# Kernel tuning notes

Measured on AMD Instinct MI355X. Metric: run time of the kernel, lower is better.

## Reference

```python
import jax, jax.numpy as jnp
import numpy as np

P_MIN = 0.8        # minimum cumulative probability mass kept per row
THRESHOLD = 1e-10  # drop matches with probability below this
EPS = 1e-6         # distance clamp (matches dist.clamp(min=1e-6) in backward)

B, N, M, D = 4, 4096, 4096, 3


def setup_inputs() -> dict:
    key = jax.random.key(0)
    kx, ky = jax.random.split(key)
    x = jax.random.normal(kx, (B, N, D), dtype=jnp.float32)
    y = jax.random.normal(ky, (B, M, D), dtype=jnp.float32)
    return {"x": x, "y": y}


def _pairwise_dist(x, y):
    # ||x_i - y_j|| via Gram trick; avoids materializing [B,N,M,D] diff tensor.
    sq = (
        jnp.sum(x * x, axis=-1)[:, :, None]
        + jnp.sum(y * y, axis=-1)[:, None, :]
        - 2.0 * jnp.einsum("bnd,bmd->bnm", x, y)
    )
    return jnp.sqrt(jnp.maximum(sq, EPS * EPS))  # [B, N, M]


def _sparse_match_weights(d):
    # Row-wise soft matching probabilities over targets j.
    p = jax.nn.softmax(-d, axis=-1)  # [B, N, M]
    # Keep the most-probable entries per row until cumulative mass reaches P_MIN
    # (the dense, jit-friendly equivalent of the COO compaction in the kernel).
    order = jnp.argsort(-p, axis=-1)
    p_sorted = jnp.take_along_axis(p, order, axis=-1)
    csum = jnp.cumsum(p_sorted, axis=-1)
    keep_sorted = (csum - p_sorted) < P_MIN  # include entry that crosses P_MIN
    inv = jnp.argsort(order, axis=-1)
    keep = jnp.take_along_axis(keep_sorted, inv, axis=-1)
    return jnp.where(keep & (p > THRESHOLD), p, 0.0)  # sparse COO values, dense layout


def reference(x, y):
    d = _pairwise_dist(x, y)                     # [B, N, M]
    w = jax.lax.stop_gradient(_sparse_match_weights(d))  # weights are constants in bwd
    loss = jnp.sum(w * d)                        # scalar matching loss
    return loss
```

## Files before the change

kernel.cpp:

```cpp
#include <hip/hip_runtime.h>


#define MCOLS 4096
#define KPT   64
#define WPB   4
#define P_MIN 0.8f

template <int CTRL, int RM, int BM, bool BC>
__device__ __forceinline__ float dpp_mov0(float x) {
    return __int_as_float(__builtin_amdgcn_update_dpp(
        0, __float_as_int(x), CTRL, RM, BM, BC));
}
__device__ __forceinline__ float dppSum(float v) {
    v += dpp_mov0<0x111, 0xF, 0xF, true >(v);
    v += dpp_mov0<0x112, 0xF, 0xF, true >(v);
    v += dpp_mov0<0x114, 0xF, 0xF, true >(v);
    v += dpp_mov0<0x118, 0xF, 0xF, true >(v);
    v += dpp_mov0<0x142, 0xA, 0xF, false>(v);
    v += dpp_mov0<0x143, 0xC, 0xF, false>(v);
    return __int_as_float(__builtin_amdgcn_readlane(__float_as_int(v), 63));
}
__device__ __forceinline__ float dppMax(float v) {
    v = fmaxf(v, dpp_mov0<0x111, 0xF, 0xF, true >(v));
    v = fmaxf(v, dpp_mov0<0x112, 0xF, 0xF, true >(v));
    v = fmaxf(v, dpp_mov0<0x114, 0xF, 0xF, true >(v));
    v = fmaxf(v, dpp_mov0<0x118, 0xF, 0xF, true >(v));
    v = fmaxf(v, dpp_mov0<0x142, 0xA, 0xF, false>(v));
    v = fmaxf(v, dpp_mov0<0x143, 0xC, 0xF, false>(v));
    return __int_as_float(__builtin_amdgcn_readlane(__float_as_int(v), 63));
}

__global__ __launch_bounds__(WPB * 64) void apml_row_wave(
        const float* __restrict__ x, const float* __restrict__ y,
        float* __restrict__ out) {
    __shared__ __align__(16) float scomp[WPB * 256];
    __shared__ float wacc[WPB];

    const int tid  = threadIdx.x;
    const int wid  = tid >> 6;
    const int lane = tid & 63;
    const int row  = blockIdx.x * WPB + wid;
    const int b    = row >> 12;

    const float x0 = x[row * 3 + 0];
    const float x1 = x[row * 3 + 1];
    const float x2 = x[row * 3 + 2];
    const float* yb = y + (size_t)b * MCOLS * 3;

    float p[KPT];
    float zl = 0.0f, pml = 0.0f;
    #pragma unroll
    for (int k = 0; k < KPT; ++k) {
        const int j = k * 64 + lane;
        const float y0 = yb[j * 3 + 0];
        const float y1 = yb[j * 3 + 1];
        const float y2 = yb[j * 3 + 2];
        const float dx = x0 - y0, dy = x1 - y1, dz = x2 - y2;
        const float sq = fmaxf(dx * dx + dy * dy + dz * dz, 1e-12f);
        const float pk = __expf(-sqrtf(sq));
        p[k] = pk;
        zl  += pk;
        pml  = fmaxf(pml, pk);
    }
    const float Z    = dppSum(zl);
    const float pmax = dppMax(pml);
    const float target = P_MIN * Z;
    const float pTop = __uint_as_float(__float_as_uint(pmax) + 1u);

    float ssl = 0.0f, ssh = pTop;
    {
        float eGl = 16.0f * dppSum(p[0] + p[1] + p[2] + p[3]);
        float eGh = 0.0f;
        for (int it = 0; it < 5; ++it) {
            float s;
            if (it & 1) {
                s = 0.5f * (ssl + ssh);
            } else {
                const float den = fmaxf(eGl - eGh, 1e-30f);
                s = ssl + (ssh - ssl) * ((eGl - target) / den);
            }
            if (!(s > ssl && s < ssh)) s = 0.5f * (ssl + ssh);
            if (!(s > ssl && s < ssh)) break;
            float m = 0.0f;
            #pragma unroll
            for (int q = 0; q < 4; ++q) m += (p[q] >= s) ? p[q] : 0.0f;
            m = 16.0f * dppSum(m);
            if (m >= target) { ssl = s; eGl = m; }
            else             { ssh = s; eGh = m; }
        }
    }

    float sl = 0.0f, sh = pTop;
    float Gl = Z,    Gh = 0.0f;
    int   Cl = MCOLS, Ch = 0;

    for (int it = 0; it < 12 && (Cl - Ch) > 256; ++it) {
        float s;
        if      (it == 0) s = ssl;
        else if (it == 1) s = ssh;
        else if (it & 1)  s = 0.5f * (sl + sh);
        else {
            const float den = fmaxf(Gl - Gh, 1e-30f);
            s = sl + (sh - sl) * ((Gl - target) / den);
        }
        if (!(s > sl && s < sh)) s = 0.5f * (sl + sh);
        if (!(s > sl && s < sh)) break;

        float m = 0.0f;
        int   c = 0;
        #pragma unroll
        for (int k = 0; k < KPT; ++k) {
            const bool ge = (p[k] >= s);
            m += ge ? p[k] : 0.0f;
            c += (int)__popcll(__ballot(ge));
        }
        m = dppSum(m);
        if (m >= target) { sl = s; Gl = m; Cl = c; }
        else             { sh = s; Gh = m; Ch = c; }
    }

    int C = 0;
    #pragma unroll
    for (int k = 0; k < KPT; ++k) {
        const bool band = (p[k] >= sl) && (p[k] < sh);
        const unsigned long long mk = __ballot(band);
        if (band) {
            const unsigned mlo = (unsigned)mk, mhi = (unsigned)(mk >> 32);
            const int within = __builtin_amdgcn_mbcnt_hi(
                                   mhi, __builtin_amdgcn_mbcnt_lo(mlo, 0));
            const int pos = C + within;
            if (pos < 256) scomp[wid * 256 + pos] = p[k];
        }
        C += (int)__popcll(mk);
    }
    __builtin_amdgcn_s_waitcnt(0);
    float cp[4];
    bool  cv[4];
    #pragma unroll
    for (int q = 0; q < 4; ++q) {
        const int idx = q * 64 + lane;
        cv[q] = (idx < C) && (idx < 256);
        cp[q] = cv[q] ? scomp[wid * 256 + idx] : 0.0f;
    }

    float pstar, mb = 0.0f;
    int   cnt = 1;
    bool  haveTie;

    if (C > 256) {
        pstar = (sl > 0.0f) ? __uint_as_float(__float_as_uint(sl) - 1u) : 0.0f;
        haveTie = false;
    } else {
        float lo_s = sl, hi_s = sh, lo_G = Gl, hi_G = Gh;
        int   lo_C = Cl, hi_C = Ch;
        for (int it = 0; it < 10 && (lo_C - hi_C) > 2; ++it) {
            float s;
            if (it & 1) {
                s = 0.5f * (lo_s + hi_s);
            } else {
                const float den = fmaxf(lo_G - hi_G, 1e-30f);
                s = lo_s + (hi_s - lo_s) * ((lo_G - target) / den);
            }
            if (!(s > lo_s && s < hi_s)) s = 0.5f * (lo_s + hi_s);
            if (!(s > lo_s && s < hi_s)) break;

            float m = 0.0f;
            int   c = Ch;
            #pragma unroll
            for (int q = 0; q < 4; ++q) {
                const bool ge = cv[q] && (cp[q] >= s);
                m += ge ? cp[q] : 0.0f;
                c += (int)__popcll(__ballot(ge));
            }
            m = Gh + dppSum(m);
            if (m >= target) { lo_s = s; lo_G = m; lo_C = c; }
            else             { hi_s = s; hi_G = m; hi_C = c; }
        }

        float scur = hi_s, M = hi_G;
        bool ok = false;
        pstar = lo_s;
        for (int e = 0; e < 16; ++e) {
            float vl = 0.0f;
            #pragma unroll
            for (int q = 0; q < 4; ++q)
                vl = fmaxf(vl, (cv[q] && cp[q] < scur) ? cp[q] : 0.0f);
            const float v = dppMax(vl);
            if (!(v > 0.0f)) break;
            int cvn = 0;
            #pragma unroll
            for (int q = 0; q < 4; ++q)
                cvn += (int)__popcll(__ballot(cv[q] && (cp[q] == v)));
            const float Mn = M + v * (float)cvn;
            if (Mn >= target) { pstar = v; mb = M; cnt = cvn; ok = true; break; }
            M = Mn; scur = v;
        }
        haveTie = ok;
        if (!ok) {
            pstar = (lo_s > 0.0f) ? __uint_as_float(__float_as_uint(lo_s) - 1u)
                                  : 0.0f;
        }
    }

    float spd = 0.0f;
    #pragma unroll
    for (int k = 0; k < KPT; ++k) {
        const float t = (p[k] > pstar) ? p[k] : 1.0f;
        spd += t * (-__logf(t));
    }
    spd = dppSum(spd);

    if (lane == 0) {
        float tie = 0.0f;
        if (haveTie) {
            const float R = (target - mb) / pstar;
            int q = (int)ceilf(R);
            if (q < 1) q = 1;
            if (q > cnt) q = cnt;
            tie = (float)q * pstar * (-__logf(pstar));
        }
        wacc[wid] = (spd + tie) / Z;
    }
    __syncthreads();
    if (tid == 0) {
        atomicAdd(out, wacc[0] + wacc[1] + wacc[2] + wacc[3]);
    }
}

extern "C" void kernel_launch(void* const* d_in, const int* in_sizes, int n_in,
                              void* d_out, int out_size, void* d_ws, size_t ws_size,
                              hipStream_t stream) {
    const float* x = (const float*)d_in[0];
    const float* y = (const float*)d_in[1];
    float* out = (float*)d_out;

    const int nrows = in_sizes[0] / 3;
    const int nblocks = nrows / WPB;

    hipMemsetAsync(out, 0, sizeof(float), stream);
    apml_row_wave<<<nblocks, WPB * 64, 0, stream>>>(x, y, out);
}
```

Baseline: 166.9 us.

## Restructure threshold search with multi-probe passes and larger compaction buffer

Replaces the serial secant/bisection threshold search over the full row with a single pass that tests four bracketing thresholds around the sampled estimate at once. It also doubles the compaction capacity to 512 entries and refines inside it with two-threshold probes per iteration. The max-reduction is dropped by fixing the upper bound at 1.0, and the sample estimate now uses 8 columns instead of 4. The aim is fewer serial full-row passes and reductions, at the cost of more register pressure and more work per pass.

New measurement: 205.4 us. 23.0% more time.

```diff
diff --git a/kernel.cpp b/kernel.cpp
--- a/kernel.cpp
+++ b/kernel.cpp
@@ -5,6 +5,7 @@
 #define KPT   64
 #define WPB   4
 #define P_MIN 0.8f
+#define CAP   512
 
 template <int CTRL, int RM, int BM, bool BC>
 __device__ __forceinline__ float dpp_mov0(float x) {
@@ -20,6 +21,34 @@
     v += dpp_mov0<0x143, 0xC, 0xF, false>(v);
     return __int_as_float(__builtin_amdgcn_readlane(__float_as_int(v), 63));
 }
+__device__ __forceinline__ void dppSum2(float& a, float& b) {
+    a += dpp_mov0<0x111, 0xF, 0xF, true >(a); b += dpp_mov0<0x111, 0xF, 0xF, true >(b);
+    a += dpp_mov0<0x112, 0xF, 0xF, true >(a); b += dpp_mov0<0x112, 0xF, 0xF, true >(b);
+    a += dpp_mov0<0x114, 0xF, 0xF, true >(a); b += dpp_mov0<0x114, 0xF, 0xF, true >(b);
+    a += dpp_mov0<0x118, 0xF, 0xF, true >(a); b += dpp_mov0<0x118, 0xF, 0xF, true >(b);
+    a += dpp_mov0<0x142, 0xA, 0xF, false>(a); b += dpp_mov0<0x142, 0xA, 0xF, false>(b);
+    a += dpp_mov0<0x143, 0xC, 0xF, false>(a); b += dpp_mov0<0x143, 0xC, 0xF, false>(b);
+    a = __int_as_float(__builtin_amdgcn_readlane(__float_as_int(a), 63));
+    b = __int_as_float(__builtin_amdgcn_readlane(__float_as_int(b), 63));
+}
+__device__ __forceinline__ void dppSum4(float& a, float& b, float& c, float& d) {
+    a += dpp_mov0<0x111, 0xF, 0xF, true >(a); b += dpp_mov0<0x111, 0xF, 0xF, true >(b);
+    c += dpp_mov0<0x111, 0xF, 0xF, true >(c); d += dpp_mov0<0x111, 0xF, 0xF, true >(d);
+    a += dpp_mov0<0x112, 0xF, 0xF, true >(a); b += dpp_mov0<0x112, 0xF, 0xF, true >(b);
+    c += dpp_mov0<0x112, 0xF, 0xF, true >(c); d += dpp_mov0<0x112, 0xF, 0xF, true >(d);
+    a += dpp_mov0<0x114, 0xF, 0xF, true >(a); b += dpp_mov0<0x114, 0xF, 0xF, true >(b);
+    c += dpp_mov0<0x114, 0xF, 0xF, true >(c); d += dpp_mov0<0x114, 0xF, 0xF, true >(d);
+    a += dpp_mov0<0x118, 0xF, 0xF, true >(a); b += dpp_mov0<0x118, 0xF, 0xF, true >(b);
+    c += dpp_mov0<0x118, 0xF, 0xF, true >(c); d += dpp_mov0<0x118, 0xF, 0xF, true >(d);
+    a += dpp_mov0<0x142, 0xA, 0xF, false>(a); b += dpp_mov0<0x142, 0xA, 0xF, false>(b);
+    c += dpp_mov0<0x142, 0xA, 0xF, false>(c); d += dpp_mov0<0x142, 0xA, 0xF, false>(d);
+    a += dpp_mov0<0x143, 0xC, 0xF, false>(a); b += dpp_mov0<0x143, 0xC, 0xF, false>(b);
+    c += dpp_mov0<0x143, 0xC, 0xF, false>(c); d += dpp_mov0<0x143, 0xC, 0xF, false>(d);
+    a = __int_as_float(__builtin_amdgcn_readlane(__float_as_int(a), 63));
+    b = __int_as_float(__builtin_amdgcn_readlane(__float_as_int(b), 63));
+    c = __int_as_float(__builtin_amdgcn_readlane(__float_as_int(c), 63));
+    d = __int_as_float(__builtin_amdgcn_readlane(__float_as_int(d), 63));
+}
 __device__ __forceinline__ float dppMax(float v) {
     v = fmaxf(v, dpp_mov0<0x111, 0xF, 0xF, true >(v));
     v = fmaxf(v, dpp_mov0<0x112, 0xF, 0xF, true >(v));
@@ -33,7 +62,7 @@
 __global__ __launch_bounds__(WPB * 64) void apml_row_wave(
         const float* __restrict__ x, const float* __restrict__ y,
         float* __restrict__ out) {
-    __shared__ __align__(16) float scomp[WPB * 256];
+    __shared__ __align__(16) float scomp[WPB * CAP];
     __shared__ float wacc[WPB];
 
     const int tid  = threadIdx.x;
@@ -48,7 +77,7 @@
     const float* yb = y + (size_t)b * MCOLS * 3;
 
     float p[KPT];
-    float zl = 0.0f, pml = 0.0f;
+    float zl = 0.0f;
     #pragma unroll
     for (int k = 0; k < KPT; ++k) {
         const int j = k * 64 + lane;
@@ -60,18 +89,19 @@
         const float pk = __expf(-sqrtf(sq));
         p[k] = pk;
         zl  += pk;
-        pml  = fmaxf(pml, pk);
-    }
-    const float Z    = dppSum(zl);
-    const float pmax = dppMax(pml);
+    }
+    const float Z      = dppSum(zl);
     const float target = P_MIN * Z;
-    const float pTop = __uint_as_float(__float_as_uint(pmax) + 1u);
+    const float pTop   = 1.0f;
 
     float ssl = 0.0f, ssh = pTop;
     {
-        float eGl = 16.0f * dppSum(p[0] + p[1] + p[2] + p[3]);
+        float ea = 0.0f, eb = 0.0f;
+        #pragma unroll
+        for (int q = 0; q < 8; q += 2) { ea += p[q]; eb += p[q + 1]; }
+        float eGl = 8.0f * dppSum(ea + eb);
         float eGh = 0.0f;
-        for (int it = 0; it < 5; ++it) {
+        for (int it = 0; it < 6; ++it) {
             float s;
             if (it & 1) {
                 s = 0.5f * (ssl + ssh);
@@ -81,25 +111,51 @@
             }
             if (!(s > ssl && s < ssh)) s = 0.5f * (ssl + ssh);
             if (!(s > ssl && s < ssh)) break;
-            float m = 0.0f;
+            float ma = 0.0f, mb2 = 0.0f;
             #pragma unroll
-            for (int q = 0; q < 4; ++q) m += (p[q] >= s) ? p[q] : 0.0f;
-            m = 16.0f * dppSum(m);
+            for (int q = 0; q < 8; q += 2) {
+                ma  += (p[q]     >= s) ? p[q]     : 0.0f;
+                mb2 += (p[q + 1] >= s) ? p[q + 1] : 0.0f;
+            }
+            const float m = 8.0f * dppSum(ma + mb2);
             if (m >= target) { ssl = s; eGl = m; }
             else             { ssh = s; eGh = m; }
         }
     }
 
-    float sl = 0.0f, sh = pTop;
-    float Gl = Z,    Gh = 0.0f;
-    int   Cl = MCOLS, Ch = 0;
-
-    for (int it = 0; it < 12 && (Cl - Ch) > 256; ++it) {
+    const float wdu = ssh - ssl;
+    const float u1  = fmaxf(ssl, 1e-30f);
+    const float u0  = fmaxf(ssl - wdu, 0.5f * u1);
+    const float u2  = ssh;
+    const float u3  = fminf(ssh + wdu, pTop);
+
+    float m0 = 0.0f, m1 = 0.0f, m2 = 0.0f, m3 = 0.0f;
+    int   c0 = 0,    c1 = 0,    c2 = 0,    c3 = 0;
+    #pragma unroll
+    for (int k = 0; k < KPT; ++k) {
+        const float pk = p[k];
+        const bool g0 = (pk >= u0), g1 = (pk >= u1);
+        const bool g2 = (pk >= u2), g3 = (pk >= u3);
+        m0 += g0 ? pk : 0.0f; c0 += (int)__popcll(__ballot(g0));
+        m1 += g1 ? pk : 0.0f; c1 += (int)__popcll(__ballot(g1));
+        m2 += g2 ? pk : 0.0f; c2 += (int)__popcll(__ballot(g2));
+        m3 += g3 ? pk : 0.0f; c3 += (int)__popcll(__ballot(g3));
+    }
+    dppSum4(m0, m1, m2, m3);
+
+    float sl, sh, Gl, Gh;
+    int   Cl, Ch;
+    if      (m3 >= target) { sl = u3;   Gl = m3; Cl = c3;    sh = pTop; Gh = 0.0f; Ch = 0;  }
+    else if (m2 >= target) { sl = u2;   Gl = m2; Cl = c2;    sh = u3;   Gh = m3;   Ch = c3; }
+    else if (m1 >= target) { sl = u1;   Gl = m1; Cl = c1;    sh = u2;   Gh = m2;   Ch = c2; }
+    else if (m0 >= target) { sl = u0;   Gl = m0; Cl = c0;    sh = u1;   Gh = m1;   Ch = c1; }
+    else                   { sl = 0.0f; Gl = Z;  Cl = MCOLS; sh = u0;   Gh = m0;   Ch = c0; }
+
+    for (int it = 0; it < 8 && (Cl - Ch) > CAP; ++it) {
         float s;
-        if      (it == 0) s = ssl;
-        else if (it == 1) s = ssh;
-        else if (it & 1)  s = 0.5f * (sl + sh);
-        else {
+        if (it & 1) {
+            s = 0.5f * (sl + sh);
+        } else {
             const float den = fmaxf(Gl - Gh, 1e-30f);
             s = sl + (sh - sl) * ((Gl - target) / den);
         }
@@ -119,7 +175,7 @@
         else             { sh = s; Gh = m; Ch = c; }
     }
 
-    int C = 0;
+    int Cb = 0;
     #pragma unroll
     for (int k = 0; k < KPT; ++k) {
         const bool band = (p[k] >= sl) && (p[k] < sh);
@@ -128,71 +184,74 @@
             const unsigned mlo = (unsigned)mk, mhi = (unsigned)(mk >> 32);
             const int within = __builtin_amdgcn_mbcnt_hi(
                                    mhi, __builtin_amdgcn_mbcnt_lo(mlo, 0));
-            const int pos = C + within;
-            if (pos < 256) scomp[wid * 256 + pos] = p[k];
-        }
-        C += (int)__popcll(mk);
+            const int pos = Cb + within;
+            if (pos < CAP) scomp[wid * CAP + pos] = p[k];
+        }
+        Cb += (int)__popcll(mk);
     }
     __builtin_amdgcn_s_waitcnt(0);
-    float cp[4];
-    bool  cv[4];
-    #pragma unroll
-    for (int q = 0; q < 4; ++q) {
+    const int Cc = (Cb < CAP) ? Cb : CAP;
+    float cp[8];
+    #pragma unroll
+    for (int q = 0; q < 8; ++q) {
         const int idx = q * 64 + lane;
-        cv[q] = (idx < C) && (idx < 256);
-        cp[q] = cv[q] ? scomp[wid * 256 + idx] : 0.0f;
-    }
-
-    float pstar, mb = 0.0f;
+        cp[q] = (idx < Cc) ? scomp[wid * CAP + idx] : 0.0f;
+    }
+
+    float pstar, mbv = 0.0f;
     int   cnt = 1;
     bool  haveTie;
 
-    if (C > 256) {
+    if (Cb > CAP) {
         pstar = (sl > 0.0f) ? __uint_as_float(__float_as_uint(sl) - 1u) : 0.0f;
         haveTie = false;
     } else {
         float lo_s = sl, hi_s = sh, lo_G = Gl, hi_G = Gh;
         int   lo_C = Cl, hi_C = Ch;
-        for (int it = 0; it < 10 && (lo_C - hi_C) > 2; ++it) {
-            float s;
-            if (it & 1) {
-                s = 0.5f * (lo_s + hi_s);
-            } else {
-                const float den = fmaxf(lo_G - hi_G, 1e-30f);
-                s = lo_s + (hi_s - lo_s) * ((lo_G - target) / den);
+        for (int it = 0; it < 6 && (lo_C - hi_C) > 2; ++it) {
+            const float sB = 0.5f * (lo_s + hi_s);
+            if (!(sB > lo_s && sB < hi_s)) break;
+            float sA = lo_s + (hi_s - lo_s) *
+                       ((lo_G - target) / fmaxf(lo_G - hi_G, 1e-30f));
+            if (!(sA > lo_s && sA < hi_s)) sA = sB;
+            const float t0 = fminf(sA, sB), t1 = fmaxf(sA, sB);
+
+            float a0 = 0.0f, a1 = 0.0f;
+            int   k0 = 0,    k1 = 0;
+            #pragma unroll
+            for (int q = 0; q < 8; ++q) {
+                const bool g0 = (cp[q] >= t0);
+                const bool g1 = (cp[q] >= t1);
+                a0 += g0 ? cp[q] : 0.0f; k0 += (int)__popcll(__ballot(g0));
+                a1 += g1 ? cp[q] : 0.0f; k1 += (int)__popcll(__ballot(g1));
             }
-            if (!(s > lo_s && s < hi_s)) s = 0.5f * (lo_s + hi_s);
-            if (!(s > lo_s && s < hi_s)) break;
-
-            float m = 0.0f;
-            int   c = Ch;
-            #pragma unroll
-            for (int q = 0; q < 4; ++q) {
-                const bool ge = cv[q] && (cp[q] >= s);
-                m += ge ? cp[q] : 0.0f;
-                c += (int)__popcll(__ballot(ge));
-            }
-            m = Gh + dppSum(m);
-            if (m >= target) { lo_s = s; lo_G = m; lo_C = c; }
-            else             { hi_s = s; hi_G = m; hi_C = c; }
+            dppSum2(a0, a1);
+            const float M0 = Gh + a0, M1 = Gh + a1;
+            const int   D0 = Ch + k0, D1 = Ch + k1;
+            if      (M1 >= target) { lo_s = t1; lo_G = M1; lo_C = D1; }
+            else if (M0 >= target) { lo_s = t0; lo_G = M0; lo_C = D0;
+                                     hi_s = t1; hi_G = M1; hi_C = D1; }
+            else                   { hi_s = t0; hi_G = M0; hi_C = D0; }
         }
 
         float scur = hi_s, M = hi_G;
         bool ok = false;
         pstar = lo_s;
         for (int e = 0; e < 16; ++e) {
-            float vl = 0.0f;
+            float v0 = 0.0f, v1 = 0.0f;
             #pragma unroll
-            for (int q = 0; q < 4; ++q)
-                vl = fmaxf(vl, (cv[q] && cp[q] < scur) ? cp[q] : 0.0f);
-            const float v = dppMax(vl);
+            for (int q = 0; q < 8; q += 2) {
+                v0 = fmaxf(v0, (cp[q]     < scur) ? cp[q]     : 0.0f);
+                v1 = fmaxf(v1, (cp[q + 1] < scur) ? cp[q + 1] : 0.0f);
+            }
+            const float v = dppMax(fmaxf(v0, v1));
             if (!(v > 0.0f)) break;
             int cvn = 0;
             #pragma unroll
-            for (int q = 0; q < 4; ++q)
-                cvn += (int)__popcll(__ballot(cv[q] && (cp[q] == v)));
+            for (int q = 0; q < 8; ++q)
+                cvn += (int)__popcll(__ballot(cp[q] == v));
             const float Mn = M + v * (float)cvn;
-            if (Mn >= target) { pstar = v; mb = M; cnt = cvn; ok = true; break; }
+            if (Mn >= target) { pstar = v; mbv = M; cnt = cvn; ok = true; break; }
             M = Mn; scur = v;
         }
         haveTie = ok;
@@ -213,7 +272,7 @@
     if (lane == 0) {
         float tie = 0.0f;
         if (haveTie) {
-            const float R = (target - mb) / pstar;
+            const float R = (target - mbv) / pstar;
             int q = (int)ceilf(R);
             if (q < 1) q = 1;
             if (q > cnt) q = cnt;
```
